# Kernel tuning notes

Measured on AMD Instinct MI355X. Metric: run time of the kernel, lower is better.

The kernel has to match this reference:

```python
import jax, jax.numpy as jnp
import numpy as np

N = 50000        # nodes
E = 800000       # edges (avg degree 16)
C_IN = 128       # in_channels
H = 64           # hidden (state is [N, 2H])
NC = 40          # num_classes
L = 15           # layers
DT = 0.1         # dt
JAC = 2          # jacobi_steps
LN_EPS = 1e-5


def setup_inputs() -> dict:
    key = jax.random.key(0)
    ks = jax.random.split(key, 8)
    x = jax.random.normal(ks[0], (N, C_IN), dtype=jnp.float32)
    edge_index = jax.random.randint(ks[1], (2, E), 0, N, dtype=jnp.int64)
    lift_w = jax.random.normal(ks[2], (H, C_IN), dtype=jnp.float32) * 0.05
    lift_b = jnp.zeros((H,), dtype=jnp.float32)
    # per-layer LVConv scalars (init at alpha0/beta0/dx0/dy0) and residual gates
    alpha = jnp.full((L,), 0.2, dtype=jnp.float32)
    beta = jnp.full((L,), 0.1, dtype=jnp.float32)
    dx = jnp.full((L,), 0.15, dtype=jnp.float32)
    dy = jnp.full((L,), 0.8, dtype=jnp.float32)
    tau = jnp.full((L,), 0.7, dtype=jnp.float32)
    ln_w = jnp.ones((L, 2 * H), dtype=jnp.float32)
    ln_b = jnp.zeros((L, 2 * H), dtype=jnp.float32)
    out_w = jax.random.normal(ks[3], (NC, H), dtype=jnp.float32) * 0.05
    out_b = jnp.zeros((NC,), dtype=jnp.float32)
    logit_scale = jnp.array(2.5, dtype=jnp.float32)
    return {"x": x, "edge_index": edge_index, "lift_w": lift_w, "lift_b": lift_b,
            "alpha": alpha, "beta": beta, "dx": dx, "dy": dy, "tau": tau,
            "ln_w": ln_w, "ln_b": ln_b, "out_w": out_w, "out_b": out_b,
            "logit_scale": logit_scale}


def reference(x, edge_index, lift_w, lift_b, alpha, beta, dx, dy, tau,
              ln_w, ln_b, out_w, out_b, logit_scale):
    src, dst = edge_index[0], edge_index[1]
    # symmetric GCN edge weights: deg^-1/2[src] * deg^-1/2[dst]
    deg = jax.ops.segment_sum(jnp.ones((E,), x.dtype), dst, num_segments=N)
    dinv = jax.lax.rsqrt(jnp.maximum(deg, 1.0))
    ew = dinv[src] * dinv[dst]                       # [E]

    def spmm(Z):  # A_hat @ Z via gather/scatter-add, Z: [N, H]
        return jax.ops.segment_sum(ew[:, None] * Z[src], dst, num_segments=N)

    X0 = jnp.tanh(x @ lift_w.T + lift_b)             # [N, H]
    h = jnp.concatenate([X0, jnp.ones_like(X0)], -1)  # [N, 2H], Y0 = ones

    def jacobi(rhs, d):
        # solve (I + DT*d*(I - A_hat)) Z = rhs; diag of L is 1 (sym norm)
        diag = 1.0 + DT * d
        Z = rhs / diag
        for _ in range(JAC):
            Z = (rhs + DT * d * spmm(Z)) / diag
        return Z

    def layer(h, p):
        a, b, dxl, dyl, t, lw, lb = p
        X, Y = h[:, :H], h[:, H:]
        XY = X * Y
        rhsX = X + DT * (a * X - b * XY)   # prey reaction
        rhsY = Y + DT * (b * XY - a * Y)   # predator reaction
        h_hat = jnp.concatenate([jacobi(rhsX, dxl), jacobi(rhsY, dyl)], -1)
        g = jax.nn.sigmoid(t)
        h = (1.0 - g) * h + g * h_hat      # sigmoid-gated residual
        mu = jnp.mean(h, -1, keepdims=True)
        var = jnp.var(h, -1, keepdims=True)
        h = (h - mu) * jax.lax.rsqrt(var + LN_EPS) * lw + lb
        return h, None

    h, _ = jax.lax.scan(layer, h, (alpha, beta, dx, dy, tau, ln_w, ln_b))
    X = h[:, :H]                                      # use_x_only
    return (logit_scale * X) @ out_w.T + out_b        # [N, NC]
```

## Files before the change

### kernel.cpp

```cpp
#include <hip/hip_runtime.h>
#include <hip/hip_fp16.h>

#define NN 50000
#define NE 800000
#define CIN 128
#define HH 64
#define NCLS 40
#define NL 15
#define DTC 0.1f
#define LNEPS 1e-5f
#define NB_SCAN 196

typedef float f32x2 __attribute__((ext_vector_type(2)));


__device__ inline unsigned pack_bf2(float x, float y) {
    unsigned ux = __float_as_uint(x);
    unsigned uy = __float_as_uint(y);
    ux = (ux + 0x7fffu + ((ux >> 16) & 1u)) >> 16;
    uy = (uy + 0x7fffu + ((uy >> 16) & 1u)) >> 16;
    return ux | (uy << 16);
}
__device__ inline float2 unpack_bf2(unsigned p) {
    float2 r;
    r.x = __uint_as_float(p << 16);
    r.y = __uint_as_float(p & 0xffff0000u);
    return r;
}
__device__ inline unsigned pack_h2(float x, float y) {
    __half2 h = __floats2half2_rn(x, y);
    return *reinterpret_cast<unsigned*>(&h);
}
__device__ inline float2 unpack_h2(unsigned p) {
    __half2 h = *reinterpret_cast<__half2*>(&p);
    return __half22float2(h);
}
__device__ inline unsigned short pack_fp8x2(float x, float y) {
    int r = __builtin_amdgcn_cvt_pk_fp8_f32(x, y, 0, false);
    return (unsigned short)(r & 0xffff);
}
__device__ inline float2 unpack_fp8x2(unsigned short p) {
    f32x2 v = __builtin_amdgcn_cvt_pk_f32_fp8((int)(unsigned)p, false);
    float2 r; r.x = v.x; r.y = v.y; return r;
}


__global__ __launch_bounds__(256) void k_deg(const int* __restrict__ dst, int* __restrict__ deg) {
    int e = blockIdx.x * 256 + threadIdx.x;
    if (e < NE) atomicAdd(&deg[dst[e]], 1);
}

__global__ __launch_bounds__(256) void k_scan1(const int* __restrict__ deg, int* __restrict__ rp,
                                               int* __restrict__ bsum, float* __restrict__ dinv) {
    int i = blockIdx.x * 256 + threadIdx.x;
    int v = (i < NN) ? deg[i] : 0;
    if (i < NN) dinv[i] = rsqrtf(fmaxf((float)v, 1.0f));
    int lane = threadIdx.x & 63, wid = threadIdx.x >> 6;
    int inc = v;
#pragma unroll
    for (int d = 1; d < 64; d <<= 1) {
        int t = __shfl_up(inc, d, 64);
        if (lane >= d) inc += t;
    }
    __shared__ int wsum[4];
    if (lane == 63) wsum[wid] = inc;
    __syncthreads();
    int woff = 0;
#pragma unroll
    for (int w = 0; w < 4; ++w)
        if (w < wid) woff += wsum[w];
    if (i < NN) rp[i] = woff + inc - v;
    if (threadIdx.x == 255) bsum[blockIdx.x] = woff + inc;
}

__global__ __launch_bounds__(256) void k_scan2(const int* __restrict__ bsum, int* __restrict__ boff) {
    int t = threadIdx.x;
    int v = (t < NB_SCAN) ? bsum[t] : 0;
    int lane = t & 63, wid = t >> 6;
    int inc = v;
#pragma unroll
    for (int d = 1; d < 64; d <<= 1) {
        int tt = __shfl_up(inc, d, 64);
        if (lane >= d) inc += tt;
    }
    __shared__ int wsum[4];
    if (lane == 63) wsum[wid] = inc;
    __syncthreads();
    int woff = 0;
#pragma unroll
    for (int w = 0; w < 4; ++w)
        if (w < wid) woff += wsum[w];
    boff[t] = woff + inc - v;
}

__global__ __launch_bounds__(256) void k_scan3(int* __restrict__ rp, const int* __restrict__ boff) {
    int i = blockIdx.x * 256 + threadIdx.x;
    if (i < NN) rp[i] += boff[i >> 8];
    else if (i == NN) rp[NN] = NE;
}

__global__ __launch_bounds__(256) void k_scatter(const int* __restrict__ src, const int* __restrict__ dst,
                                                 const float* __restrict__ dinv, const int* __restrict__ rp,
                                                 int* __restrict__ cnt, uint2* __restrict__ edges) {
    int e = blockIdx.x * 256 + threadIdx.x;
    if (e >= NE) return;
    int s = src[e], d = dst[e];
    int pos = rp[d] + atomicAdd(&cnt[d], 1);
    uint2 rec;
    rec.x = (unsigned)s * 128u;
    rec.y = __float_as_uint(dinv[s] * dinv[d]);
    edges[pos] = rec;
}


#define LIFT_NPB 16

__global__ __launch_bounds__(256) void k_lift(const float* __restrict__ x, const float* __restrict__ lw,
                                              const float* __restrict__ lb,
                                              const float* __restrict__ alpha, const float* __restrict__ beta,
                                              const float* __restrict__ dxp, const float* __restrict__ dyp,
                                              unsigned* __restrict__ hpk, unsigned short* __restrict__ z0bf8) {
    __shared__ unsigned Wt2[CIN / 2][HH + 1];
    __shared__ float xs[LIFT_NPB][CIN];
    int t = threadIdx.x;
    for (int idx = t; idx < (CIN / 2) * HH; idx += 256) {
        int c = idx & 63, kk = idx >> 6;
        Wt2[kk][c] = pack_bf2(lw[c * CIN + 2 * kk], lw[c * CIN + 2 * kk + 1]);
    }
    int n0 = blockIdx.x * LIFT_NPB;
#pragma unroll
    for (int i = 0; i < LIFT_NPB * CIN / 256; ++i) {
        int idx = i * 256 + t;
        int r = idx >> 7, c = idx & 127;
        xs[r][c] = x[(size_t)(n0 + r) * CIN + c];
    }
    __syncthreads();
    int lane = t & 63, wid = t >> 6;
    float bias = lb[lane];
    float a = alpha[0], b = beta[0];
    float idx0 = 1.0f / (1.0f + DTC * dxp[0]);
    float idy0 = 1.0f / (1.0f + DTC * dyp[0]);
    const float2* x0 = (const float2*)&xs[wid * 4 + 0][0];
    const float2* x1 = (const float2*)&xs[wid * 4 + 1][0];
    const float2* x2 = (const float2*)&xs[wid * 4 + 2][0];
    const float2* x3 = (const float2*)&xs[wid * 4 + 3][0];
    float ac0 = 0.f, ac1 = 0.f, ac2 = 0.f, ac3 = 0.f;
#pragma unroll 8
    for (int kk = 0; kk < CIN / 2; ++kk) {
        float2 wv = unpack_bf2(Wt2[kk][lane]);
        float2 v0 = x0[kk], v1 = x1[kk], v2 = x2[kk], v3 = x3[kk];
        ac0 = fmaf(v0.y, wv.y, fmaf(v0.x, wv.x, ac0));
        ac1 = fmaf(v1.y, wv.y, fmaf(v1.x, wv.x, ac1));
        ac2 = fmaf(v2.y, wv.y, fmaf(v2.x, wv.x, ac2));
        ac3 = fmaf(v3.y, wv.y, fmaf(v3.x, wv.x, ac3));
    }
#pragma unroll
    for (int i = 0; i < 4; ++i) {
        float acc = i == 0 ? ac0 : i == 1 ? ac1 : i == 2 ? ac2 : ac3;
        float hx = tanhf(bias + acc);
        int n = n0 + wid * 4 + i;
        hpk[(size_t)n * HH + lane] = pack_h2(hx, 1.0f);
        float rx = hx + DTC * (a * hx - b * hx);
        float ry = 1.0f + DTC * (b * hx - a);
        z0bf8[(size_t)n * HH + lane] = pack_fp8x2(rx * idx0, ry * idy0);
    }
}


#define GLOAD(g, q, comp) unsigned short g = *(const unsigned short*)(base + q.comp + lane2)
#define CONS(g, q, wcomp, aX, aY)                                      \
    do {                                                               \
        float2 v = unpack_fp8x2(g);                                    \
        float w = __uint_as_float(q.wcomp);                            \
        aX = fmaf(w, v.x, aX);                                         \
        aY = fmaf(w, v.y, aY);                                         \
    } while (0)

__device__ __forceinline__ void batchAB(const char* __restrict__ base, const uint2* __restrict__ edges,
                                        int eA, int eB, int lane2,
                                        float& aXA, float& aYA, float& aXB, float& aYB) {
    uint4 qa0 = *(const uint4*)(edges + eA);
    uint4 qa1 = *(const uint4*)(edges + eA + 2);
    uint4 qa2 = *(const uint4*)(edges + eA + 4);
    uint4 qa3 = *(const uint4*)(edges + eA + 6);
    uint4 qb0 = *(const uint4*)(edges + eB);
    uint4 qb1 = *(const uint4*)(edges + eB + 2);
    uint4 qb2 = *(const uint4*)(edges + eB + 4);
    uint4 qb3 = *(const uint4*)(edges + eB + 6);
    GLOAD(ga0, qa0, x); GLOAD(ga1, qa0, z);
    GLOAD(ga2, qa1, x); GLOAD(ga3, qa1, z);
    GLOAD(ga4, qa2, x); GLOAD(ga5, qa2, z);
    GLOAD(ga6, qa3, x); GLOAD(ga7, qa3, z);
    GLOAD(gb0, qb0, x); GLOAD(gb1, qb0, z);
    GLOAD(gb2, qb1, x); GLOAD(gb3, qb1, z);
    GLOAD(gb4, qb2, x); GLOAD(gb5, qb2, z);
    GLOAD(gb6, qb3, x); GLOAD(gb7, qb3, z);
    CONS(ga0, qa0, y, aXA, aYA); CONS(ga1, qa0, w, aXA, aYA);
    CONS(ga2, qa1, y, aXA, aYA); CONS(ga3, qa1, w, aXA, aYA);
    CONS(ga4, qa2, y, aXA, aYA); CONS(ga5, qa2, w, aXA, aYA);
    CONS(ga6, qa3, y, aXA, aYA); CONS(ga7, qa3, w, aXA, aYA);
    CONS(gb0, qb0, y, aXB, aYB); CONS(gb1, qb0, w, aXB, aYB);
    CONS(gb2, qb1, y, aXB, aYB); CONS(gb3, qb1, w, aXB, aYB);
    CONS(gb4, qb2, y, aXB, aYB); CONS(gb5, qb2, w, aXB, aYB);
    CONS(gb6, qb3, y, aXB, aYB); CONS(gb7, qb3, w, aXB, aYB);
}

__device__ __forceinline__ void batch8(const char* __restrict__ base, const uint2* __restrict__ edges,
                                       int e, int lane2, float& accX, float& accY) {
    uint4 q0 = *(const uint4*)(edges + e);
    uint4 q1 = *(const uint4*)(edges + e + 2);
    uint4 q2 = *(const uint4*)(edges + e + 4);
    uint4 q3 = *(const uint4*)(edges + e + 6);
    GLOAD(g0, q0, x); GLOAD(g1, q0, z);
    GLOAD(g2, q1, x); GLOAD(g3, q1, z);
    GLOAD(g4, q2, x); GLOAD(g5, q2, z);
    GLOAD(g6, q3, x); GLOAD(g7, q3, z);
    CONS(g0, q0, y, accX, accY); CONS(g1, q0, w, accX, accY);
    CONS(g2, q1, y, accX, accY); CONS(g3, q1, w, accX, accY);
    CONS(g4, q2, y, accX, accY); CONS(g5, q2, w, accX, accY);
    CONS(g6, q3, y, accX, accY); CONS(g7, q3, w, accX, accY);
}

__device__ __forceinline__ void edge_one(const char* __restrict__ base, const uint2* __restrict__ edges,
                                         int e, int lane2, float& accX, float& accY) {
    uint2 ed = edges[e];
    float w = __uint_as_float(ed.y);
    float2 v = unpack_fp8x2(*(const unsigned short*)(base + ed.x + lane2));
    accX = fmaf(w, v.x, accX);
    accY = fmaf(w, v.y, accY);
}

__device__ __forceinline__ void gather2(const unsigned short* __restrict__ srcbuf,
                                        const uint2* __restrict__ edges,
                                        int e0A, int e1A, int e0B, int e1B, int lane2,
                                        float& aXA, float& aYA, float& aXB, float& aYB) {
    const char* base = (const char*)srcbuf;
    int eA = e0A, eB = e0B;
    if ((eA & 1) && eA < e1A) { edge_one(base, edges, eA, lane2, aXA, aYA); ++eA; }
    if ((eB & 1) && eB < e1B) { edge_one(base, edges, eB, lane2, aXB, aYB); ++eB; }
    while (eA + 8 <= e1A && eB + 8 <= e1B) {
        batchAB(base, edges, eA, eB, lane2, aXA, aYA, aXB, aYB);
        eA += 8; eB += 8;
    }
    while (eA + 8 <= e1A) { batch8(base, edges, eA, lane2, aXA, aYA); eA += 8; }
    while (eB + 8 <= e1B) { batch8(base, edges, eB, lane2, aXB, aYB); eB += 8; }
    for (; eA < e1A; ++eA) edge_one(base, edges, eA, lane2, aXA, aYA);
    for (; eB < e1B; ++eB) edge_one(base, edges, eB, lane2, aXB, aYB);
}


__global__ __launch_bounds__(256) void k_phase1(const unsigned short* __restrict__ z0bf8,
                                                unsigned short* __restrict__ z1bf8,
                                                const int* __restrict__ rp, const uint2* __restrict__ edges,
                                                const float* __restrict__ dxp, const float* __restrict__ dyp,
                                                int l) {
    int lane = threadIdx.x & 63, wid = threadIdx.x >> 6;
    int nA = blockIdx.x * 8 + wid * 2;
    int nB = nA + 1;
    float dx = dxp[l], dy = dyp[l];
    float cx = DTC * dx / (1.0f + DTC * dx);
    float cy = DTC * dy / (1.0f + DTC * dy);
    int e0A = __builtin_amdgcn_readfirstlane(rp[nA]);
    int e1A = __builtin_amdgcn_readfirstlane(rp[nA + 1]);
    int e1B = __builtin_amdgcn_readfirstlane(rp[nA + 2]);
    float aXA = 0.f, aYA = 0.f, aXB = 0.f, aYB = 0.f;
    gather2(z0bf8, edges, e0A, e1A, e1A, e1B, lane * 2, aXA, aYA, aXB, aYB);
    float2 zA = unpack_fp8x2(z0bf8[(size_t)nA * HH + lane]);
    float2 zB = unpack_fp8x2(z0bf8[(size_t)nB * HH + lane]);
    z1bf8[(size_t)nA * HH + lane] = pack_fp8x2(fmaf(cx, aXA, zA.x), fmaf(cy, aYA, zA.y));
    z1bf8[(size_t)nB * HH + lane] = pack_fp8x2(fmaf(cx, aXB, zB.x), fmaf(cy, aYB, zB.y));
}


__device__ __forceinline__ void phase2_epi(int n, int lane, float accX, float accY,
                                           unsigned* __restrict__ hpk, unsigned short* __restrict__ z0bf8,
                                           float a, float b, float idx_, float idy_, float cx, float cy,
                                           float g, const float* __restrict__ lwr, const float* __restrict__ lbr,
                                           float a2, float b2, float idx2, float idy2, bool wz0) {
    unsigned* hp = hpk + (size_t)n * HH + lane;
    float2 hv = unpack_h2(*hp);
    float hx = hv.x, hy = hv.y;
    float xy = hx * hy;
    float z0x = (hx + DTC * (a * hx - b * xy)) * idx_;
    float z0y = (hy + DTC * (b * xy - a * hy)) * idy_;
    float z2x = fmaf(cx, accX, z0x);
    float z2y = fmaf(cy, accY, z0y);
    float nx = fmaf(g, z2x - hx, hx);
    float ny = fmaf(g, z2y - hy, hy);
    float s1 = nx + ny;
    float s2 = fmaf(nx, nx, ny * ny);
#pragma unroll
    for (int m = 1; m < 64; m <<= 1) {
        s1 += __shfl_xor(s1, m, 64);
        s2 += __shfl_xor(s2, m, 64);
    }
    float mean = s1 * (1.0f / 128.0f);
    float var = fmaf(-mean, mean, s2 * (1.0f / 128.0f));
    float rstd = rsqrtf(var + LNEPS);
    float ox = fmaf((nx - mean) * rstd, lwr[lane], lbr[lane]);
    float oy = fmaf((ny - mean) * rstd, lwr[HH + lane], lbr[HH + lane]);
    *hp = pack_h2(ox, oy);
    if (wz0) {
        float xy2 = ox * oy;
        float r2x = ox + DTC * (a2 * ox - b2 * xy2);
        float r2y = oy + DTC * (b2 * xy2 - a2 * oy);
        z0bf8[(size_t)n * HH + lane] = pack_fp8x2(r2x * idx2, r2y * idy2);
    }
}

__global__ __launch_bounds__(256) void k_phase2(unsigned* __restrict__ hpk,
                                                unsigned short* __restrict__ z0bf8,
                                                const unsigned short* __restrict__ z1bf8,
                                                const int* __restrict__ rp, const uint2* __restrict__ edges,
                                                const float* __restrict__ alpha, const float* __restrict__ beta,
                                                const float* __restrict__ dxp, const float* __restrict__ dyp,
                                                const float* __restrict__ taup,
                                                const float* __restrict__ lnw, const float* __restrict__ lnb,
                                                int l) {
    int lane = threadIdx.x & 63, wid = threadIdx.x >> 6;
    int nA = blockIdx.x * 8 + wid * 2;
    int nB = nA + 1;
    float a = alpha[l], b = beta[l], dx = dxp[l], dy = dyp[l];
    float idx_ = 1.0f / (1.0f + DTC * dx);
    float idy_ = 1.0f / (1.0f + DTC * dy);
    float cx = DTC * dx * idx_, cy = DTC * dy * idy_;
    int e0A = __builtin_amdgcn_readfirstlane(rp[nA]);
    int e1A = __builtin_amdgcn_readfirstlane(rp[nA + 1]);
    int e1B = __builtin_amdgcn_readfirstlane(rp[nA + 2]);
    float aXA = 0.f, aYA = 0.f, aXB = 0.f, aYB = 0.f;
    gather2(z1bf8, edges, e0A, e1A, e1A, e1B, lane * 2, aXA, aYA, aXB, aYB);
    int l2 = (l + 1 < NL) ? l + 1 : l;
    float a2 = alpha[l2], b2 = beta[l2];
    float idx2 = 1.0f / (1.0f + DTC * dxp[l2]);
    float idy2 = 1.0f / (1.0f + DTC * dyp[l2]);
    float g = 1.0f / (1.0f + expf(-taup[l]));
    bool wz0 = (l + 1 < NL);
    const float* lwr = lnw + (size_t)l * 128;
    const float* lbr = lnb + (size_t)l * 128;
    phase2_epi(nA, lane, aXA, aYA, hpk, z0bf8, a, b, idx_, idy_, cx, cy, g, lwr, lbr, a2, b2, idx2, idy2, wz0);
    phase2_epi(nB, lane, aXB, aYB, hpk, z0bf8, a, b, idx_, idy_, cx, cy, g, lwr, lbr, a2, b2, idx2, idy2, wz0);
}


__global__ __launch_bounds__(256) void k_out(const unsigned* __restrict__ hpk, const float* __restrict__ ow,
                                             const float* __restrict__ ob, const float* __restrict__ lsp,
                                             float* __restrict__ out) {
    __shared__ float hs[64][65];
    __shared__ float ows[NCLS][65];
    __shared__ float obs[NCLS];
    int t = threadIdx.x;
    int n0 = blockIdx.x * 64;
#pragma unroll
    for (int i = 0; i < 16; ++i) {
        int idx = i * 256 + t;
        int r = idx >> 6, c = idx & 63;
        int n = n0 + r;
        hs[r][c] = (n < NN) ? unpack_h2(hpk[(size_t)n * HH + c]).x : 0.f;
    }
#pragma unroll
    for (int i = 0; i < 10; ++i) {
        int idx = i * 256 + t;
        int j = idx >> 6, c = idx & 63;
        ows[j][c] = ow[j * HH + c];
    }
    if (t < NCLS) obs[t] = ob[t];
    __syncthreads();
    float ls = lsp[0];
#pragma unroll
    for (int i = 0; i < 10; ++i) {
        int o = i * 256 + t;
        int nl = o / NCLS;
        int j = o - nl * NCLS;
        float acc = 0.f;
#pragma unroll 8
        for (int k = 0; k < HH; ++k) acc = fmaf(hs[nl][k], ows[j][k], acc);
        int n = n0 + nl;
        if (n < NN) out[(size_t)n * NCLS + j] = fmaf(ls, acc, obs[j]);
    }
}


extern "C" void kernel_launch(void* const* d_in, const int* in_sizes, int n_in,
                              void* d_out, int out_size, void* d_ws, size_t ws_size,
                              hipStream_t stream) {
    const float* x     = (const float*)d_in[0];
    const int*   ei    = (const int*)d_in[1];
    const float* lw    = (const float*)d_in[2];
    const float* lb    = (const float*)d_in[3];
    const float* alpha = (const float*)d_in[4];
    const float* beta  = (const float*)d_in[5];
    const float* dxp   = (const float*)d_in[6];
    const float* dyp   = (const float*)d_in[7];
    const float* taup  = (const float*)d_in[8];
    const float* lnw   = (const float*)d_in[9];
    const float* lnb   = (const float*)d_in[10];
    const float* ow    = (const float*)d_in[11];
    const float* ob    = (const float*)d_in[12];
    const float* lsp   = (const float*)d_in[13];
    float* out = (float*)d_out;

    const int* srcp = ei;
    const int* dstp = ei + NE;

    char* ws = (char*)d_ws;
    size_t o = 0;
    auto alloc = [&](size_t b) { size_t r = o; o += (b + 255) & ~(size_t)255; return r; };
    int*            row_ptr = (int*)(ws + alloc((NN + 1) * sizeof(int)));
    int*            deg     = (int*)(ws + alloc(NN * sizeof(int)));
    int*            cnt     = (int*)(ws + alloc(NN * sizeof(int)));
    float*          dinv    = (float*)(ws + alloc(NN * sizeof(float)));
    int*            bsum    = (int*)(ws + alloc(256 * sizeof(int)));
    int*            boff    = (int*)(ws + alloc(256 * sizeof(int)));
    uint2*          edges   = (uint2*)(ws + alloc((size_t)NE * sizeof(uint2)));
    unsigned*       hpk     = (unsigned*)(ws + alloc((size_t)NN * HH * sizeof(unsigned)));
    unsigned short* z0bf8   = (unsigned short*)(ws + alloc((size_t)NN * HH * sizeof(unsigned short)));
    unsigned short* z1bf8   = (unsigned short*)(ws + alloc((size_t)NN * HH * sizeof(unsigned short)));

    hipMemsetAsync(deg, 0, NN * sizeof(int), stream);
    hipMemsetAsync(cnt, 0, NN * sizeof(int), stream);

    k_deg<<<(NE + 255) / 256, 256, 0, stream>>>(dstp, deg);
    k_scan1<<<NB_SCAN, 256, 0, stream>>>(deg, row_ptr, bsum, dinv);
    k_scan2<<<1, 256, 0, stream>>>(bsum, boff);
    k_scan3<<<NB_SCAN, 256, 0, stream>>>(row_ptr, boff);
    k_scatter<<<(NE + 255) / 256, 256, 0, stream>>>(srcp, dstp, dinv, row_ptr, cnt, edges);

    k_lift<<<NN / LIFT_NPB, 256, 0, stream>>>(x, lw, lb, alpha, beta, dxp, dyp, hpk, z0bf8);

    for (int l = 0; l < NL; ++l) {
        k_phase1<<<NN / 8, 256, 0, stream>>>(z0bf8, z1bf8, row_ptr, edges, dxp, dyp, l);
        k_phase2<<<NN / 8, 256, 0, stream>>>(hpk, z0bf8, z1bf8, row_ptr, edges,
                                             alpha, beta, dxp, dyp, taup, lnw, lnb, l);
    }

    k_out<<<(NN + 63) / 64, 256, 0, stream>>>(hpk, ow, ob, lsp, out);
}
```

Before: 980.0 us.

## Split phase-1 SpMM into two channel-half passes with two edges per wave

```diff
diff --git a/kernel.cpp b/kernel.cpp
--- a/kernel.cpp
+++ b/kernel.cpp
@@ -163,6 +163,80 @@
         float rx = hx + DTC * (a * hx - b * hx);
         float ry = 1.0f + DTC * (b * hx - a);
         z0bf8[(size_t)n * HH + lane] = pack_fp8x2(rx * idx0, ry * idy0);
+    }
+}
+
+
+__device__ __forceinline__ void p1_cons(unsigned short g, float w, float& aX, float& aY) {
+    float2 v = unpack_fp8x2(g);
+    aX = fmaf(w, v.x, aX);
+    aY = fmaf(w, v.y, aY);
+}
+
+__global__ __launch_bounds__(256) void k_phase1h(const unsigned short* __restrict__ z0bf8,
+                                                 unsigned short* __restrict__ z1bf8,
+                                                 const int* __restrict__ rp, const uint2* __restrict__ edges,
+                                                 const float* __restrict__ dxp, const float* __restrict__ dyp,
+                                                 int l, int pass) {
+    int lane = threadIdx.x & 63, wid = threadIdx.x >> 6;
+    int n = blockIdx.x * 4 + wid;
+    bool hi = (lane >> 5) != 0;
+    int lh = lane & 31;
+    float dx = dxp[l], dy = dyp[l];
+    float cx = DTC * dx / (1.0f + DTC * dx);
+    float cy = DTC * dy / (1.0f + DTC * dy);
+    int e0 = __builtin_amdgcn_readfirstlane(rp[n]);
+    int e1 = __builtin_amdgcn_readfirstlane(rp[n + 1]);
+    const char* base = (const char*)z0bf8 + pass * 64;
+    int choff = lh * 2;
+    float aX = 0.f, aY = 0.f;
+    int e = e0;
+    for (; e + 16 <= e1; e += 16) {
+        uint4 q0 = *(const uint4*)(edges + e);
+        uint4 q1 = *(const uint4*)(edges + e + 2);
+        uint4 q2 = *(const uint4*)(edges + e + 4);
+        uint4 q3 = *(const uint4*)(edges + e + 6);
+        uint4 q4 = *(const uint4*)(edges + e + 8);
+        uint4 q5 = *(const uint4*)(edges + e + 10);
+        uint4 q6 = *(const uint4*)(edges + e + 12);
+        uint4 q7 = *(const uint4*)(edges + e + 14);
+        unsigned o0 = hi ? q0.z : q0.x, o1 = hi ? q1.z : q1.x;
+        unsigned o2 = hi ? q2.z : q2.x, o3 = hi ? q3.z : q3.x;
+        unsigned o4 = hi ? q4.z : q4.x, o5 = hi ? q5.z : q5.x;
+        unsigned o6 = hi ? q6.z : q6.x, o7 = hi ? q7.z : q7.x;
+        unsigned short g0 = *(const unsigned short*)(base + o0 + choff);
+        unsigned short g1 = *(const unsigned short*)(base + o1 + choff);
+        unsigned short g2 = *(const unsigned short*)(base + o2 + choff);
+        unsigned short g3 = *(const unsigned short*)(base + o3 + choff);
+        unsigned short g4 = *(const unsigned short*)(base + o4 + choff);
+        unsigned short g5 = *(const unsigned short*)(base + o5 + choff);
+        unsigned short g6 = *(const unsigned short*)(base + o6 + choff);
+        unsigned short g7 = *(const unsigned short*)(base + o7 + choff);
+        p1_cons(g0, __uint_as_float(hi ? q0.w : q0.y), aX, aY);
+        p1_cons(g1, __uint_as_float(hi ? q1.w : q1.y), aX, aY);
+        p1_cons(g2, __uint_as_float(hi ? q2.w : q2.y), aX, aY);
+        p1_cons(g3, __uint_as_float(hi ? q3.w : q3.y), aX, aY);
+        p1_cons(g4, __uint_as_float(hi ? q4.w : q4.y), aX, aY);
+        p1_cons(g5, __uint_as_float(hi ? q5.w : q5.y), aX, aY);
+        p1_cons(g6, __uint_as_float(hi ? q6.w : q6.y), aX, aY);
+        p1_cons(g7, __uint_as_float(hi ? q7.w : q7.y), aX, aY);
+    }
+    for (; e < e1; e += 2) {
+        uint2 rA = edges[e];
+        bool vB = (e + 1 < e1);
+        uint2 rB = vB ? edges[e + 1] : rA;
+        unsigned wBbits = vB ? rB.y : 0u;
+        unsigned off = hi ? rB.x : rA.x;
+        float w = __uint_as_float(hi ? wBbits : rA.y);
+        unsigned short g = *(const unsigned short*)(base + off + choff);
+        p1_cons(g, w, aX, aY);
+    }
+    aX += __shfl_xor(aX, 32, 64);
+    aY += __shfl_xor(aY, 32, 64);
+    if (!hi) {
+        size_t idx = (size_t)n * HH + pass * 32 + lh;
+        float2 z0 = unpack_fp8x2(z0bf8[idx]);
+        z1bf8[idx] = pack_fp8x2(fmaf(cx, aX, z0.x), fmaf(cy, aY, z0.y));
     }
 }
 
@@ -246,29 +320,6 @@
     while (eB + 8 <= e1B) { batch8(base, edges, eB, lane2, aXB, aYB); eB += 8; }
     for (; eA < e1A; ++eA) edge_one(base, edges, eA, lane2, aXA, aYA);
     for (; eB < e1B; ++eB) edge_one(base, edges, eB, lane2, aXB, aYB);
-}
-
-
-__global__ __launch_bounds__(256) void k_phase1(const unsigned short* __restrict__ z0bf8,
-                                                unsigned short* __restrict__ z1bf8,
-                                                const int* __restrict__ rp, const uint2* __restrict__ edges,
-                                                const float* __restrict__ dxp, const float* __restrict__ dyp,
-                                                int l) {
-    int lane = threadIdx.x & 63, wid = threadIdx.x >> 6;
-    int nA = blockIdx.x * 8 + wid * 2;
-    int nB = nA + 1;
-    float dx = dxp[l], dy = dyp[l];
-    float cx = DTC * dx / (1.0f + DTC * dx);
-    float cy = DTC * dy / (1.0f + DTC * dy);
-    int e0A = __builtin_amdgcn_readfirstlane(rp[nA]);
-    int e1A = __builtin_amdgcn_readfirstlane(rp[nA + 1]);
-    int e1B = __builtin_amdgcn_readfirstlane(rp[nA + 2]);
-    float aXA = 0.f, aYA = 0.f, aXB = 0.f, aYB = 0.f;
-    gather2(z0bf8, edges, e0A, e1A, e1A, e1B, lane * 2, aXA, aYA, aXB, aYB);
-    float2 zA = unpack_fp8x2(z0bf8[(size_t)nA * HH + lane]);
-    float2 zB = unpack_fp8x2(z0bf8[(size_t)nB * HH + lane]);
-    z1bf8[(size_t)nA * HH + lane] = pack_fp8x2(fmaf(cx, aXA, zA.x), fmaf(cy, aYA, zA.y));
-    z1bf8[(size_t)nB * HH + lane] = pack_fp8x2(fmaf(cx, aXB, zB.x), fmaf(cy, aYB, zB.y));
 }
 
 
@@ -428,7 +479,8 @@
     k_lift<<<NN / LIFT_NPB, 256, 0, stream>>>(x, lw, lb, alpha, beta, dxp, dyp, hpk, z0bf8);
 
     for (int l = 0; l < NL; ++l) {
-        k_phase1<<<NN / 8, 256, 0, stream>>>(z0bf8, z1bf8, row_ptr, edges, dxp, dyp, l);
+        k_phase1h<<<NN / 4, 256, 0, stream>>>(z0bf8, z1bf8, row_ptr, edges, dxp, dyp, l, 0);
+        k_phase1h<<<NN / 4, 256, 0, stream>>>(z0bf8, z1bf8, row_ptr, edges, dxp, dyp, l, 1);
         k_phase2<<<NN / 8, 256, 0, stream>>>(hpk, z0bf8, z1bf8, row_ptr, edges,
                                              alpha, beta, dxp, dyp, taup, lnw, lnb, l);
     }
```

Measured after the change: 1.384 ms. 1.41x slower.
